# Optimization experiments

Hardware: AMD Instinct MI355X
Metric: run time of the kernel (lower is better)

Reference implementation:

```python
import jax, jax.numpy as jnp
import numpy as np

N = 50000
NEG_SLOPE = 0.2


def add_self_loops(edge_index, n):
    loop = jnp.arange(n, dtype=edge_index.dtype)
    return jnp.concatenate([edge_index, jnp.stack([loop, loop])], axis=1)


def gatv2_conv(x, edge_index, Wl, bl, Wr, br, att, bias):
    """PyG GATv2Conv (share_weights=False, concat=True, add_self_loops applied by caller).
    x: [N, Fin]; edge_index: [2, E] with row0=src(j), row1=dst(i); att: [H, D].
    Returns (out [N, H*D], alpha [E, H])."""
    src, dst = edge_index[0], edge_index[1]
    H, D = att.shape
    n = x.shape[0]
    xl = (x @ Wl + bl).reshape(n, H, D)   # source-side transform
    xr = (x @ Wr + br).reshape(n, H, D)   # target-side transform
    e = jax.nn.leaky_relu(xl[src] + xr[dst], NEG_SLOPE)        # [E, H, D]
    logit = jnp.einsum('ehd,hd->eh', e, att)                    # [E, H]
    # segment softmax over edges grouped by target node
    lmax = jax.ops.segment_max(logit, dst, num_segments=n)      # [N, H]
    ex = jnp.exp(logit - lmax[dst])
    denom = jax.ops.segment_sum(ex, dst, num_segments=n)
    alpha = ex / denom[dst]                                     # [E, H]
    out = jax.ops.segment_sum(alpha[:, :, None] * xl[src], dst, num_segments=n)  # [N, H, D]
    return out.reshape(n, H * D) + bias, alpha


def setup_inputs() -> dict:
    key = jax.random.key(0)
    ks = jax.random.split(key, 16)
    E = 400000
    x = jax.random.normal(ks[0], (N, 23), dtype=jnp.float32)
    edge_index = jax.random.randint(ks[1], (2, E), 0, N, dtype=jnp.int64)
    H1, D1 = 8, 64
    F1 = H1 * D1  # 512
    s = 0.1
    return {
        'x': x,
        'edge_index': edge_index,
        'Wl1': jax.random.normal(ks[2], (23, F1), dtype=jnp.float32) * s,
        'bl1': jnp.zeros((F1,), jnp.float32),
        'Wr1': jax.random.normal(ks[3], (23, F1), dtype=jnp.float32) * s,
        'br1': jnp.zeros((F1,), jnp.float32),
        'att1': jax.random.normal(ks[4], (H1, D1), dtype=jnp.float32) * s,
        'bias1': jnp.zeros((F1,), jnp.float32),
        'Wl2': jax.random.normal(ks[5], (F1, 1), dtype=jnp.float32) * s,
        'bl2': jnp.zeros((1,), jnp.float32),
        'Wr2': jax.random.normal(ks[6], (F1, 1), dtype=jnp.float32) * s,
        'br2': jnp.zeros((1,), jnp.float32),
        'att2': jax.random.normal(ks[7], (1, 1), dtype=jnp.float32) * s,
        'bias2': jnp.zeros((1,), jnp.float32),
    }


def reference(x, edge_index, Wl1, bl1, Wr1, br1, att1, bias1,
              Wl2, bl2, Wr2, br2, att2, bias2):
    ei = add_self_loops(edge_index, N)
    h, _ = gatv2_conv(x, ei, Wl1, bl1, Wr1, br1, att1, bias1)
    h = jax.nn.relu(h)
    h, alpha = gatv2_conv(h, ei, Wl2, bl2, Wr2, br2, att2, bias2)
    return h, alpha
```

## Files before the change

### kernel.cpp

```cpp
#include <hip/hip_runtime.h>
#include <math.h>

#define NN 50000
#define E0 400000
#define EE 450000
#define FF 512
#define G1 2048
#define NPB ((NN + G1 - 1) / G1)
#define WAVES_TOTAL (G1 * 4)

__device__ __forceinline__ float leaky(float v) { return fmaxf(v, 0.2f * v); }
__device__ __forceinline__ float blo(unsigned u) { return __uint_as_float(u << 16); }
__device__ __forceinline__ float bhi(unsigned u) { return __uint_as_float(u & 0xffff0000u); }
__device__ __forceinline__ unsigned bpack(float a, float b) {
    unsigned ua = __float_as_uint(a); ua = (ua + 0x7fffu + ((ua >> 16) & 1u)) >> 16;
    unsigned ub = __float_as_uint(b); ub = (ub + 0x7fffu + ((ub >> 16) & 1u)) >> 16;
    return ua | (ub << 16);
}

__global__ __launch_bounds__(256) void k_pre(
    const float* __restrict__ x,
    const float* __restrict__ Wl1, const float* __restrict__ bl1,
    const float* __restrict__ Wr1, const float* __restrict__ br1,
    unsigned* __restrict__ xlb, unsigned* __restrict__ xrb)
{
    int t = threadIdx.x;
    int c0 = 2 * t, c1 = 2 * t + 1;
    float wl0[23], wl1v[23], wr0[23], wr1v[23];
#pragma unroll
    for (int r = 0; r < 23; r++) {
        wl0[r]  = Wl1[r * FF + c0];
        wl1v[r] = Wl1[r * FF + c1];
        wr0[r]  = Wr1[r * FF + c0];
        wr1v[r] = Wr1[r * FF + c1];
    }
    float bl0 = bl1[c0], bl1s = bl1[c1];
    float br0 = br1[c0], br1s = br1[c1];

    int i0 = blockIdx.x * NPB;
    int i1 = i0 + NPB; if (i1 > NN) i1 = NN;
    for (int i = i0; i < i1; i++) {
        int ib = __builtin_amdgcn_readfirstlane(i);
        float a0 = bl0, a1 = bl1s, b0 = br0, b1 = br1s;
#pragma unroll
        for (int r = 0; r < 23; r++) {
            float xv = x[ib * 23 + r];
            a0 += xv * wl0[r];
            a1 += xv * wl1v[r];
            b0 += xv * wr0[r];
            b1 += xv * wr1v[r];
        }
        xlb[(size_t)i * 256 + t] = bpack(a0, a1);
        xrb[(size_t)i * 256 + t] = bpack(b0, b1);
    }
}

__global__ void k_deg(const int* __restrict__ ei, int* __restrict__ deg)
{
    int e = blockIdx.x * blockDim.x + threadIdx.x;
    if (e >= EE) return;
    int dst = (e < E0) ? ei[E0 + e] : (e - E0);
    atomicAdd(&deg[dst], 1);
}

__global__ __launch_bounds__(256) void k_scan1(const int* __restrict__ deg,
                                               int* __restrict__ excl, int* __restrict__ bsum)
{
    __shared__ int wsum[4];
    int b = blockIdx.x, t = threadIdx.x;
    int base = b * 1024 + t * 4;
    int v0 = (base     < NN) ? deg[base]     : 0;
    int v1 = (base + 1 < NN) ? deg[base + 1] : 0;
    int v2 = (base + 2 < NN) ? deg[base + 2] : 0;
    int v3 = (base + 3 < NN) ? deg[base + 3] : 0;
    int tsum = v0 + v1 + v2 + v3;
    int lane = t & 63, wv = t >> 6;
    int sc = tsum;
#pragma unroll
    for (int o = 1; o < 64; o <<= 1) {
        int u = __shfl_up(sc, o, 64);
        if (lane >= o) sc += u;
    }
    if (lane == 63) wsum[wv] = sc;
    __syncthreads();
    int woff = 0;
    for (int k = 0; k < wv; k++) woff += wsum[k];
    int ex = woff + sc - tsum;
    if (base     < NN) excl[base]     = ex;
    if (base + 1 < NN) excl[base + 1] = ex + v0;
    if (base + 2 < NN) excl[base + 2] = ex + v0 + v1;
    if (base + 3 < NN) excl[base + 3] = ex + v0 + v1 + v2;
    if (t == 255) bsum[b] = woff + sc;
}

__global__ void k_scan2(int* __restrict__ bsum, int* __restrict__ offs)
{
    int t = threadIdx.x;
    int v = (t < 49) ? bsum[t] : 0;
    int sc = v;
#pragma unroll
    for (int o = 1; o < 64; o <<= 1) {
        int u = __shfl_up(sc, o, 64);
        if (t >= o) sc += u;
    }
    if (t < 49) bsum[t] = sc - v;
    if (t == 63) offs[NN] = sc;
}

__global__ __launch_bounds__(256) void k_scan3(const int* __restrict__ excl,
                                               const int* __restrict__ bsum,
                                               int* __restrict__ offs, int* __restrict__ cur)
{
    int b = blockIdx.x;
    int add = bsum[b];
    int base = b * 1024 + threadIdx.x * 4;
#pragma unroll
    for (int k = 0; k < 4; k++) {
        int idx = base + k;
        if (idx < NN) {
            int v = excl[idx] + add;
            offs[idx] = v;
            cur[idx]  = v;
        }
    }
}

__global__ void k_scatter(const int* __restrict__ ei, int* __restrict__ cur,
                          int* __restrict__ src_s)
{
    int e = blockIdx.x * blockDim.x + threadIdx.x;
    if (e >= EE) return;
    int src, dst;
    if (e < E0) { src = ei[e]; dst = ei[E0 + e]; }
    else        { src = e - E0; dst = src; }
    int p = atomicAdd(&cur[dst], 1);
    src_s[p] = src;
}

__global__ __launch_bounds__(256) void k_layer1(
    const uint4* __restrict__ xlb, const uint4* __restrict__ xrb,
    const float* __restrict__ att, const float* __restrict__ bias1,
    const float* __restrict__ Wl2, const float* __restrict__ bl2,
    const float* __restrict__ Wr2, const float* __restrict__ br2,
    const int* __restrict__ offs, const int* __restrict__ src_s,
    float* __restrict__ xl2, float* __restrict__ xr2)
{
    int t = threadIdx.x;
    int l = t & 63;
    int wid = blockIdx.x * 4 + (t >> 6);

    float4 atA = ((const float4*)att)[2 * l];
    float4 atB = ((const float4*)att)[2 * l + 1];
    float bl2v = bl2[0], br2v = br2[0];

    for (int i = wid; i < NN; i += WAVES_TOTAL) {
        uint4 xq = xrb[(size_t)i * 64 + l];
        float xr0 = blo(xq.x), xr1 = bhi(xq.x), xr2v = blo(xq.y), xr3 = bhi(xq.y);
        float xr4 = blo(xq.z), xr5 = bhi(xq.z), xr6 = blo(xq.w), xr7 = bhi(xq.w);

        float s = 0.f;
        float ac0 = 0.f, ac1 = 0.f, ac2 = 0.f, ac3 = 0.f;
        float ac4 = 0.f, ac5 = 0.f, ac6 = 0.f, ac7 = 0.f;

        int beg = offs[i], deg = offs[i + 1] - beg;

        for (int cb = 0; cb < deg; cb += 64) {
            int cnt = deg - cb; if (cnt > 64) cnt = 64;
            int myj = (l < cnt) ? src_s[beg + cb + l] : 0;

            int j0 = __builtin_amdgcn_readlane(myj, 0);
            uint4 r0 = xlb[(size_t)j0 * 64 + l];
            uint4 r1 = r0;
            if (cnt > 1) {
                int j1 = __builtin_amdgcn_readlane(myj, 1);
                r1 = xlb[(size_t)j1 * 64 + l];
            }
            for (int p = 0; p < cnt; p++) {
                uint4 r2 = r0;
                if (p + 2 < cnt) {
                    int j2 = __builtin_amdgcn_readlane(myj, p + 2);
                    r2 = xlb[(size_t)j2 * 64 + l];
                }
                float v0 = blo(r0.x), v1 = bhi(r0.x), v2 = blo(r0.y), v3 = bhi(r0.y);
                float v4 = blo(r0.z), v5 = bhi(r0.z), v6 = blo(r0.w), v7 = bhi(r0.w);
                float part;
                part  = atA.x * leaky(v0 + xr0);
                part  = fmaf(atA.y, leaky(v1 + xr1), part);
                part  = fmaf(atA.z, leaky(v2 + xr2v), part);
                part  = fmaf(atA.w, leaky(v3 + xr3), part);
                part  = fmaf(atB.x, leaky(v4 + xr4), part);
                part  = fmaf(atB.y, leaky(v5 + xr5), part);
                part  = fmaf(atB.z, leaky(v6 + xr6), part);
                part  = fmaf(atB.w, leaky(v7 + xr7), part);
                part += __shfl_xor(part, 1, 64);
                part += __shfl_xor(part, 2, 64);
                part += __shfl_xor(part, 4, 64);
                float w = __expf(part);
                s += w;
                ac0 = fmaf(w, v0, ac0); ac1 = fmaf(w, v1, ac1);
                ac2 = fmaf(w, v2, ac2); ac3 = fmaf(w, v3, ac3);
                ac4 = fmaf(w, v4, ac4); ac5 = fmaf(w, v5, ac5);
                ac6 = fmaf(w, v6, ac6); ac7 = fmaf(w, v7, ac7);
                r0 = r1; r1 = r2;
            }
        }

        float inv = 1.f / s;
        float4 bA = ((const float4*)bias1)[2 * l];
        float4 bB = ((const float4*)bias1)[2 * l + 1];
        float h0 = fmaxf(fmaf(ac0, inv, bA.x), 0.f);
        float h1 = fmaxf(fmaf(ac1, inv, bA.y), 0.f);
        float h2 = fmaxf(fmaf(ac2, inv, bA.z), 0.f);
        float h3 = fmaxf(fmaf(ac3, inv, bA.w), 0.f);
        float h4 = fmaxf(fmaf(ac4, inv, bB.x), 0.f);
        float h5 = fmaxf(fmaf(ac5, inv, bB.y), 0.f);
        float h6 = fmaxf(fmaf(ac6, inv, bB.z), 0.f);
        float h7 = fmaxf(fmaf(ac7, inv, bB.w), 0.f);

        float4 wlA = ((const float4*)Wl2)[2 * l];
        float4 wlB = ((const float4*)Wl2)[2 * l + 1];
        float4 wrA = ((const float4*)Wr2)[2 * l];
        float4 wrB = ((const float4*)Wr2)[2 * l + 1];
        float pl = h0 * wlA.x + h1 * wlA.y + h2 * wlA.z + h3 * wlA.w
                 + h4 * wlB.x + h5 * wlB.y + h6 * wlB.z + h7 * wlB.w;
        float pr = h0 * wrA.x + h1 * wrA.y + h2 * wrA.z + h3 * wrA.w
                 + h4 * wrB.x + h5 * wrB.y + h6 * wrB.z + h7 * wrB.w;
#pragma unroll
        for (int o = 32; o > 0; o >>= 1) {
            pl += __shfl_xor(pl, o, 64);
            pr += __shfl_xor(pr, o, 64);
        }
        if (l == 0) {
            xl2[i] = pl + bl2v;
            xr2[i] = pr + br2v;
        }
    }
}

__global__ void k_layer2a(const float* __restrict__ xl2, const float* __restrict__ xr2,
                          const float* __restrict__ att2, const float* __restrict__ bias2,
                          const int* __restrict__ offs, const int* __restrict__ src_s,
                          float* __restrict__ out, float* __restrict__ invs)
{
    int i = blockIdx.x * blockDim.x + threadIdx.x;
    if (i >= NN) return;
    int beg = offs[i], end = offs[i + 1];
    float xri = xr2[i], a2 = att2[0];
    float s = 0.f, num = 0.f;
    for (int p = beg; p < end; p++) {
        float v = xl2[src_s[p]];
        float w = __expf(leaky(v + xri) * a2);
        s += w;
        num = fmaf(w, v, num);
    }
    out[i] = num / s + bias2[0];
    invs[i] = 1.f / s;
}

__global__ void k_layer2b(const float* __restrict__ xl2, const float* __restrict__ xr2,
                          const float* __restrict__ att2, const int* __restrict__ ei,
                          const float* __restrict__ invs, float* __restrict__ out)
{
    int e = blockIdx.x * blockDim.x + threadIdx.x;
    if (e >= EE) return;
    int src, dst;
    if (e < E0) { src = ei[e]; dst = ei[E0 + e]; }
    else        { src = e - E0; dst = src; }
    float l = leaky(xl2[src] + xr2[dst]) * att2[0];
    out[NN + e] = __expf(l) * invs[dst];
}

extern "C" void kernel_launch(void* const* d_in, const int* in_sizes, int n_in,
                              void* d_out, int out_size, void* d_ws, size_t ws_size,
                              hipStream_t stream)
{
    const float* x     = (const float*)d_in[0];
    const int*   ei    = (const int*)d_in[1];
    const float* Wl1   = (const float*)d_in[2];
    const float* bl1   = (const float*)d_in[3];
    const float* Wr1   = (const float*)d_in[4];
    const float* br1   = (const float*)d_in[5];
    const float* att1  = (const float*)d_in[6];
    const float* bias1 = (const float*)d_in[7];
    const float* Wl2   = (const float*)d_in[8];
    const float* bl2   = (const float*)d_in[9];
    const float* Wr2   = (const float*)d_in[10];
    const float* br2   = (const float*)d_in[11];
    const float* att2  = (const float*)d_in[12];
    const float* bias2 = (const float*)d_in[13];
    float* out = (float*)d_out;

    char* ws = (char*)d_ws;
    unsigned* xlb = (unsigned*)ws; ws += (size_t)NN * 256 * 4;
    unsigned* xrb = (unsigned*)ws; ws += (size_t)NN * 256 * 4;
    float* xl2  = (float*)ws;      ws += (size_t)NN * 4;
    float* xr2  = (float*)ws;      ws += (size_t)NN * 4;
    float* invs = (float*)ws;      ws += (size_t)NN * 4;
    int* deg    = (int*)ws;        ws += (size_t)NN * 4;
    int* excl   = (int*)ws;        ws += (size_t)NN * 4;
    int* offs   = (int*)ws;        ws += (size_t)(NN + 1) * 4;
    int* cur    = (int*)ws;        ws += (size_t)NN * 4;
    int* bsum   = (int*)ws;        ws += (size_t)64 * 4;
    int* src_s  = (int*)ws;        ws += (size_t)EE * 4;

    hipMemsetAsync(deg, 0, (size_t)NN * 4, stream);

    k_pre<<<G1, 256, 0, stream>>>(x, Wl1, bl1, Wr1, br1, xlb, xrb);
    k_deg<<<(EE + 255) / 256, 256, 0, stream>>>(ei, deg);
    k_scan1<<<49, 256, 0, stream>>>(deg, excl, bsum);
    k_scan2<<<1, 64, 0, stream>>>(bsum, offs);
    k_scan3<<<49, 256, 0, stream>>>(excl, bsum, offs, cur);
    k_scatter<<<(EE + 255) / 256, 256, 0, stream>>>(ei, cur, src_s);
    k_layer1<<<G1, 256, 0, stream>>>((const uint4*)xlb, (const uint4*)xrb,
                                     att1, bias1, Wl2, bl2, Wr2, br2,
                                     offs, src_s, xl2, xr2);
    k_layer2a<<<(NN + 255) / 256, 256, 0, stream>>>(xl2, xr2, att2, bias2,
                                                    offs, src_s, out, invs);
    k_layer2b<<<(EE + 255) / 256, 256, 0, stream>>>(xl2, xr2, att2, ei, invs, out);
}
```

Before: 266.4 us.

## Fuse degree count into precompute, single-pass scan, merged layer-2, deeper prefetch

Folds degree counting into the layer-1 precompute kernel and replaces the three-kernel scan with one kernel that chains block totals through flags. Layer 2 becomes one kernel that writes alpha through a stored edge-id permutation. Layer 1 prefetches four neighbours ahead instead of two, and exp2 with pre-scaled weights replaces exp. These cut launch count and some memory traffic, but add the eid array and scattered alpha writes, and the scan relies on all 49 blocks being resident at once.

```diff
diff --git a/kernel.cpp b/kernel.cpp
--- a/kernel.cpp
+++ b/kernel.cpp
@@ -7,7 +7,10 @@
 #define FF 512
 #define G1 2048
 #define NPB ((NN + G1 - 1) / G1)
+#define EPB ((EE + G1 - 1) / G1)
 #define WAVES_TOTAL (G1 * 4)
+#define SCANB 49
+#define LOG2E 1.44269504f
 
 __device__ __forceinline__ float leaky(float v) { return fmaxf(v, 0.2f * v); }
 __device__ __forceinline__ float blo(unsigned u) { return __uint_as_float(u << 16); }
@@ -18,13 +21,24 @@
     return ua | (ub << 16);
 }
 
-__global__ __launch_bounds__(256) void k_pre(
+__global__ __launch_bounds__(256) void k_predeg(
     const float* __restrict__ x,
     const float* __restrict__ Wl1, const float* __restrict__ bl1,
     const float* __restrict__ Wr1, const float* __restrict__ br1,
-    unsigned* __restrict__ xlb, unsigned* __restrict__ xrb)
-{
-    int t = threadIdx.x;
+    const int* __restrict__ ei,
+    unsigned* __restrict__ xlb, unsigned* __restrict__ xrb, int* __restrict__ deg)
+{
+    int b = blockIdx.x, t = threadIdx.x;
+
+    {
+        int e = b * EPB + t;
+        int e1 = b * EPB + EPB; if (e1 > EE) e1 = EE;
+        if (t < EPB && e < e1) {
+            int dst = (e < E0) ? ei[E0 + e] : (e - E0);
+            atomicAdd(&deg[dst], 1);
+        }
+    }
+
     int c0 = 2 * t, c1 = 2 * t + 1;
     float wl0[23], wl1v[23], wr0[23], wr1v[23];
 #pragma unroll
@@ -37,7 +51,7 @@
     float bl0 = bl1[c0], bl1s = bl1[c1];
     float br0 = br1[c0], br1s = br1[c1];
 
-    int i0 = blockIdx.x * NPB;
+    int i0 = b * NPB;
     int i1 = i0 + NPB; if (i1 > NN) i1 = NN;
     for (int i = i0; i < i1; i++) {
         int ib = __builtin_amdgcn_readfirstlane(i);
@@ -55,18 +69,12 @@
     }
 }
 
-__global__ void k_deg(const int* __restrict__ ei, int* __restrict__ deg)
-{
-    int e = blockIdx.x * blockDim.x + threadIdx.x;
-    if (e >= EE) return;
-    int dst = (e < E0) ? ei[E0 + e] : (e - E0);
-    atomicAdd(&deg[dst], 1);
-}
-
-__global__ __launch_bounds__(256) void k_scan1(const int* __restrict__ deg,
-                                               int* __restrict__ excl, int* __restrict__ bsum)
+__global__ __launch_bounds__(256) void k_scan(
+    const int* __restrict__ deg, unsigned* __restrict__ flag,
+    int* __restrict__ offs, int* __restrict__ cur)
 {
     __shared__ int wsum[4];
+    __shared__ int s_prev;
     int b = blockIdx.x, t = threadIdx.x;
     int base = b * 1024 + t * 4;
     int v0 = (base     < NN) ? deg[base]     : 0;
@@ -85,48 +93,32 @@
     __syncthreads();
     int woff = 0;
     for (int k = 0; k < wv; k++) woff += wsum[k];
-    int ex = woff + sc - tsum;
-    if (base     < NN) excl[base]     = ex;
-    if (base + 1 < NN) excl[base + 1] = ex + v0;
-    if (base + 2 < NN) excl[base + 2] = ex + v0 + v1;
-    if (base + 3 < NN) excl[base + 3] = ex + v0 + v1 + v2;
-    if (t == 255) bsum[b] = woff + sc;
-}
-
-__global__ void k_scan2(int* __restrict__ bsum, int* __restrict__ offs)
-{
-    int t = threadIdx.x;
-    int v = (t < 49) ? bsum[t] : 0;
-    int sc = v;
-#pragma unroll
-    for (int o = 1; o < 64; o <<= 1) {
-        int u = __shfl_up(sc, o, 64);
-        if (t >= o) sc += u;
-    }
-    if (t < 49) bsum[t] = sc - v;
-    if (t == 63) offs[NN] = sc;
-}
-
-__global__ __launch_bounds__(256) void k_scan3(const int* __restrict__ excl,
-                                               const int* __restrict__ bsum,
-                                               int* __restrict__ offs, int* __restrict__ cur)
-{
-    int b = blockIdx.x;
-    int add = bsum[b];
-    int base = b * 1024 + threadIdx.x * 4;
-#pragma unroll
-    for (int k = 0; k < 4; k++) {
-        int idx = base + k;
-        if (idx < NN) {
-            int v = excl[idx] + add;
-            offs[idx] = v;
-            cur[idx]  = v;
-        }
-    }
+    int btot = wsum[0] + wsum[1] + wsum[2] + wsum[3];
+
+    if (t == 0) atomicExch(&flag[b], (unsigned)btot + 1u);
+    int contrib = 0;
+    if (t < b) {
+        unsigned f;
+        do { f = atomicAdd(&flag[t], 0u); } while (f == 0u);
+        contrib = (int)(f - 1u);
+    }
+    if (t < 64) {
+#pragma unroll
+        for (int o = 32; o > 0; o >>= 1) contrib += __shfl_xor(contrib, o, 64);
+        if (t == 0) s_prev = contrib;
+    }
+    __syncthreads();
+    int add = s_prev;
+    int ex = add + woff + sc - tsum;
+    if (base     < NN) { offs[base]     = ex;                cur[base]     = ex; }
+    if (base + 1 < NN) { offs[base + 1] = ex + v0;           cur[base + 1] = ex + v0; }
+    if (base + 2 < NN) { offs[base + 2] = ex + v0 + v1;      cur[base + 2] = ex + v0 + v1; }
+    if (base + 3 < NN) { offs[base + 3] = ex + v0 + v1 + v2; cur[base + 3] = ex + v0 + v1 + v2; }
+    if (b == SCANB - 1 && t == 255) offs[NN] = add + btot;
 }
 
 __global__ void k_scatter(const int* __restrict__ ei, int* __restrict__ cur,
-                          int* __restrict__ src_s)
+                          int* __restrict__ src_s, int* __restrict__ eid_s)
 {
     int e = blockIdx.x * blockDim.x + threadIdx.x;
     if (e >= EE) return;
@@ -135,6 +127,7 @@
     else        { src = e - E0; dst = src; }
     int p = atomicAdd(&cur[dst], 1);
     src_s[p] = src;
+    eid_s[p] = e;
 }
 
 __global__ __launch_bounds__(256) void k_layer1(
@@ -151,6 +144,8 @@
 
     float4 atA = ((const float4*)att)[2 * l];
     float4 atB = ((const float4*)att)[2 * l + 1];
+    atA.x *= LOG2E; atA.y *= LOG2E; atA.z *= LOG2E; atA.w *= LOG2E;
+    atB.x *= LOG2E; atB.y *= LOG2E; atB.z *= LOG2E; atB.w *= LOG2E;
     float bl2v = bl2[0], br2v = br2[0];
 
     for (int i = wid; i < NN; i += WAVES_TOTAL) {
@@ -170,17 +165,15 @@
 
             int j0 = __builtin_amdgcn_readlane(myj, 0);
             uint4 r0 = xlb[(size_t)j0 * 64 + l];
-            uint4 r1 = r0;
-            if (cnt > 1) {
-                int j1 = __builtin_amdgcn_readlane(myj, 1);
-                r1 = xlb[(size_t)j1 * 64 + l];
-            }
+            uint4 r1 = r0, r2 = r0, r3 = r0;
+            if (cnt > 1) r1 = xlb[(size_t)__builtin_amdgcn_readlane(myj, 1) * 64 + l];
+            if (cnt > 2) r2 = xlb[(size_t)__builtin_amdgcn_readlane(myj, 2) * 64 + l];
+            if (cnt > 3) r3 = xlb[(size_t)__builtin_amdgcn_readlane(myj, 3) * 64 + l];
+
             for (int p = 0; p < cnt; p++) {
-                uint4 r2 = r0;
-                if (p + 2 < cnt) {
-                    int j2 = __builtin_amdgcn_readlane(myj, p + 2);
-                    r2 = xlb[(size_t)j2 * 64 + l];
-                }
+                uint4 rn = r0;
+                if (p + 4 < cnt)
+                    rn = xlb[(size_t)__builtin_amdgcn_readlane(myj, p + 4) * 64 + l];
                 float v0 = blo(r0.x), v1 = bhi(r0.x), v2 = blo(r0.y), v3 = bhi(r0.y);
                 float v4 = blo(r0.z), v5 = bhi(r0.z), v6 = blo(r0.w), v7 = bhi(r0.w);
                 float part;
@@ -195,13 +188,13 @@
                 part += __shfl_xor(part, 1, 64);
                 part += __shfl_xor(part, 2, 64);
                 part += __shfl_xor(part, 4, 64);
-                float w = __expf(part);
+                float w = exp2f(part);
                 s += w;
                 ac0 = fmaf(w, v0, ac0); ac1 = fmaf(w, v1, ac1);
                 ac2 = fmaf(w, v2, ac2); ac3 = fmaf(w, v3, ac3);
                 ac4 = fmaf(w, v4, ac4); ac5 = fmaf(w, v5, ac5);
                 ac6 = fmaf(w, v6, ac6); ac7 = fmaf(w, v7, ac7);
-                r0 = r1; r1 = r2;
+                r0 = r1; r1 = r2; r2 = r3; r3 = rn;
             }
         }
 
@@ -237,37 +230,30 @@
     }
 }
 
-__global__ void k_layer2a(const float* __restrict__ xl2, const float* __restrict__ xr2,
-                          const float* __restrict__ att2, const float* __restrict__ bias2,
-                          const int* __restrict__ offs, const int* __restrict__ src_s,
-                          float* __restrict__ out, float* __restrict__ invs)
+__global__ void k_layer2(const float* __restrict__ xl2, const float* __restrict__ xr2,
+                         const float* __restrict__ att2, const float* __restrict__ bias2,
+                         const int* __restrict__ offs, const int* __restrict__ src_s,
+                         const int* __restrict__ eid_s, float* __restrict__ out)
 {
     int i = blockIdx.x * blockDim.x + threadIdx.x;
     if (i >= NN) return;
     int beg = offs[i], end = offs[i + 1];
-    float xri = xr2[i], a2 = att2[0];
+    float xri = xr2[i];
+    float a2l = att2[0] * LOG2E;
     float s = 0.f, num = 0.f;
     for (int p = beg; p < end; p++) {
         float v = xl2[src_s[p]];
-        float w = __expf(leaky(v + xri) * a2);
+        float w = exp2f(leaky(v + xri) * a2l);
         s += w;
         num = fmaf(w, v, num);
     }
     out[i] = num / s + bias2[0];
-    invs[i] = 1.f / s;
-}
-
-__global__ void k_layer2b(const float* __restrict__ xl2, const float* __restrict__ xr2,
-                          const float* __restrict__ att2, const int* __restrict__ ei,
-                          const float* __restrict__ invs, float* __restrict__ out)
-{
-    int e = blockIdx.x * blockDim.x + threadIdx.x;
-    if (e >= EE) return;
-    int src, dst;
-    if (e < E0) { src = ei[e]; dst = ei[E0 + e]; }
-    else        { src = e - E0; dst = src; }
-    float l = leaky(xl2[src] + xr2[dst]) * att2[0];
-    out[NN + e] = __expf(l) * invs[dst];
+    float inv = 1.f / s;
+    for (int p = beg; p < end; p++) {
+        float v = xl2[src_s[p]];
+        float w = exp2f(leaky(v + xri) * a2l);
+        out[NN + eid_s[p]] = w * inv;
+    }
 }
 
 extern "C" void kernel_launch(void* const* d_in, const int* in_sizes, int n_in,
@@ -295,26 +281,21 @@
     unsigned* xrb = (unsigned*)ws; ws += (size_t)NN * 256 * 4;
     float* xl2  = (float*)ws;      ws += (size_t)NN * 4;
     float* xr2  = (float*)ws;      ws += (size_t)NN * 4;
-    float* invs = (float*)ws;      ws += (size_t)NN * 4;
     int* deg    = (int*)ws;        ws += (size_t)NN * 4;
-    int* excl   = (int*)ws;        ws += (size_t)NN * 4;
+    unsigned* flag = (unsigned*)ws; ws += (size_t)64 * 4;
     int* offs   = (int*)ws;        ws += (size_t)(NN + 1) * 4;
     int* cur    = (int*)ws;        ws += (size_t)NN * 4;
-    int* bsum   = (int*)ws;        ws += (size_t)64 * 4;
     int* src_s  = (int*)ws;        ws += (size_t)EE * 4;
-
-    hipMemsetAsync(deg, 0, (size_t)NN * 4, stream);
-
-    k_pre<<<G1, 256, 0, stream>>>(x, Wl1, bl1, Wr1, br1, xlb, xrb);
-    k_deg<<<(EE + 255) / 256, 256, 0, stream>>>(ei, deg);
-    k_scan1<<<49, 256, 0, stream>>>(deg, excl, bsum);
-    k_scan2<<<1, 64, 0, stream>>>(bsum, offs);
-    k_scan3<<<49, 256, 0, stream>>>(excl, bsum, offs, cur);
-    k_scatter<<<(EE + 255) / 256, 256, 0, stream>>>(ei, cur, src_s);
+    int* eid_s  = (int*)ws;        ws += (size_t)EE * 4;
+
+    hipMemsetAsync(deg, 0, (size_t)(NN + 64) * 4, stream);
+
+    k_predeg<<<G1, 256, 0, stream>>>(x, Wl1, bl1, Wr1, br1, ei, xlb, xrb, deg);
+    k_scan<<<SCANB, 256, 0, stream>>>(deg, flag, offs, cur);
+    k_scatter<<<(EE + 255) / 256, 256, 0, stream>>>(ei, cur, src_s, eid_s);
     k_layer1<<<G1, 256, 0, stream>>>((const uint4*)xlb, (const uint4*)xrb,
                                      att1, bias1, Wl2, bl2, Wr2, br2,
                                      offs, src_s, xl2, xr2);
-    k_layer2a<<<(NN + 255) / 256, 256, 0, stream>>>(xl2, xr2, att2, bias2,
-                                                    offs, src_s, out, invs);
-    k_layer2b<<<(EE + 255) / 256, 256, 0, stream>>>(xl2, xr2, att2, ei, invs, out);
-}
+    k_layer2<<<(NN + 255) / 256, 256, 0, stream>>>(xl2, xr2, att2, bias2,
+                                                   offs, src_s, eid_s, out);
+}
```

Result: faster. 258.9 us (-2.8%).
